# Kernel tuning notes

Hardware: AMD Instinct MI355X
Metric: run time of the kernel (lower is better)

## Reference

```python
import jax, jax.numpy as jnp
import numpy as np

SCALE, K, PATCH, STRIDE = 2, 5, 3, 1
EPS = 1e-5


def im2patch(x, p, s):
    # x: (b,c,H,W) -> (b,c,p,p,m1,m2), 'VALID' patches (padding is 0 for our sizes)
    b, c, H, W = x.shape
    m1 = (H - p) // s + 1
    m2 = (W - p) // s + 1
    ii = (jnp.arange(m1) * s)[:, None] + jnp.arange(p)[None, :]   # (m1,p)
    jj = (jnp.arange(m2) * s)[:, None] + jnp.arange(p)[None, :]   # (m2,p)
    pt = x[:, :, ii[:, :, None, None], jj[None, None, :, :]]      # (b,c,m1,p,m2,p)
    return pt.transpose(0, 1, 3, 5, 2, 4)                         # (b,c,p,p,m1,m2)


def patch2im(patches, p, s):
    # overlap-add fold, averaged by per-pixel patch counts (torch F.fold / ones-fold divisor)
    b, c, _, _, m1, m2 = patches.shape
    Hp = (m1 - 1) * s + p
    Wp = (m2 - 1) * s + p
    out = jnp.zeros((b, c, Hp, Wp), patches.dtype)
    cnt = jnp.zeros((Hp, Wp), patches.dtype)
    for i in range(p):          # fixed small loop over patch offsets (p*p = 36)
        for j in range(p):
            out = out.at[:, :, i:i + s * m1:s, j:j + s * m2:s].add(patches[:, :, i, j])
            cnt = cnt.at[i:i + s * m1:s, j:j + s * m2:s].add(1.0)
    return out / cnt


def setup_inputs():
    key = jax.random.key(0)
    k1, k2, k3 = jax.random.split(key, 3)
    b, cy, H, W = 1, 64, 80, 80
    y = jax.random.normal(k1, (b, cy, H, W), jnp.float32)
    yd = jax.random.normal(k2, (b, cy * SCALE ** 2, H // SCALE, W // SCALE), jnp.float32)
    m = ((H - PATCH) // STRIDE + 1) ** 2
    n = ((H // SCALE - PATCH) // STRIDE + 1) ** 2
    idx_k = jax.random.randint(k3, (b, m, K), 0, n, jnp.int32)
    return {"y": y, "yd": yd, "idx_k": idx_k}


def reference(y, yd, idx_k):
    b, cy, H, W = y.shape
    c = yd.shape[1]           # = cy * scale^2
    rs = SCALE ** 2
    y_p = im2patch(y, PATCH, STRIDE)      # (b,cy,p,p,m1,m2)
    yd_p = im2patch(yd, PATCH, STRIDE)    # (b,c,p,p,n1,n2)
    m1, m2 = y_p.shape[-2:]
    n1, n2 = yd_p.shape[-2:]
    m, n = m1 * m2, n1 * n2
    f = c * PATCH * PATCH
    y_flat = y_p.transpose(0, 4, 5, 1, 2, 3).reshape(b, m, f // rs)
    yd_flat = yd_p.transpose(0, 4, 5, 1, 2, 3).reshape(b, n, f)
    # top-k neighbor gather: (b,n,f)[idx (b,m,k)] -> (b,m,k,f) -> (b,m,f,k)
    z = jax.vmap(lambda t, i: t[i])(yd_flat, idx_k)
    z = z.transpose(0, 1, 3, 2)
    # AdaIN: normalize gathered HR patches, apply LR query patch stats (unbiased var, torch default)
    y_n = y_flat.reshape(b, m, c // rs, PATCH * PATCH)
    z_n = z.reshape(b, m, c // rs, rs * PATCH * PATCH, K)
    z_mu = z_n.mean(axis=3, keepdims=True)
    z_sd = jnp.sqrt(z_n.var(axis=3, ddof=1, keepdims=True) + EPS)
    y_mu = y_n.mean(axis=3, keepdims=True)[..., None]        # (b,m,c',1,1)
    y_sd = jnp.sqrt(y_n.var(axis=3, ddof=1, keepdims=True) + EPS)[..., None]
    z = ((z_n - z_mu) / z_sd * y_sd + y_mu).reshape(b, m, f, K)
    # rearrange f = (cy, scale, scale, p1, p2) into SR patches (b, k*cy, p*scale, p*scale, m1, m2)
    z = z.transpose(0, 3, 2, 1)                                   # (b,k,f,m)
    z = z.reshape(b, K, cy, SCALE, SCALE, PATCH, PATCH, m1, m2)
    z = z.transpose(0, 1, 2, 5, 3, 6, 4, 7, 8)                    # (b,k,cy,p1,s,p2,s,m1,m2)
    z = z.reshape(b, K * cy, PATCH * SCALE, PATCH * SCALE, m1, m2)
    z_sr = patch2im(z, PATCH * SCALE, STRIDE * SCALE)             # (b,k*cy,H*scale,W*scale)
    return z_sr.reshape(b, K * cy, H * SCALE, W * SCALE)
```

## Files before the change

### kernel.cpp

```cpp
#include <hip/hip_runtime.h>
#include <hip/hip_fp16.h>
#include <string.h>

#define CY     64
#define HY     80
#define HD     40
#define SPD    (HD*HD)
#define M1     78
#define N1     38
#define M_TOT  (M1*M1)
#define N_TOT  (N1*N1)
#define KK     5
#define HS     160
#define EPSF   1e-5f
#define LP     33

typedef float f32x2 __attribute__((ext_vector_type(2)));

__device__ __forceinline__ unsigned pkf16(float a, float b) {
    __half2 h = __floats2half2_rn(a, b);
    unsigned u; memcpy(&u, &h, 4); return u;
}
__device__ __forceinline__ f32x2 upk2(unsigned u) {
    __half2 h; memcpy(&h, &u, 4);
    float2 f = __half22float2(h);
    f32x2 r; r.x = f.x; r.y = f.y; return r;
}

__global__ __launch_bounds__(256) void pre_kernel(const float* __restrict__ y,
                                                  const float* __restrict__ yd,
                                                  uint4* __restrict__ ydW,
                                                  unsigned* __restrict__ zstP,
                                                  unsigned* __restrict__ ystP) {
    int id = blockIdx.x * 256 + threadIdx.x;
    if (id < SPD * 64) {
        int cc = id & 63, sp = id >> 6;
        const float* b0 = yd + (cc * 4) * SPD + sp;
        int d = (sp < SPD - 1) ? 1 : 0;
        ydW[sp * 64 + cc] = make_uint4(pkf16(b0[0], b0[SPD]),
                                       pkf16(b0[2*SPD], b0[3*SPD]),
                                       pkf16(b0[d], b0[SPD+d]),
                                       pkf16(b0[2*SPD+d], b0[3*SPD+d]));
        return;
    }
    id -= SPD * 64;
    if (id < N_TOT * 64) {
        int n  = id % N_TOT;
        int cc = id / N_TOT;
        int ni = n / N1, nj = n - ni * N1;
        const float* base = yd + (cc * 4) * SPD + ni * HD + nj;
        float s = 0.f, sq = 0.f;
#pragma unroll
        for (int r = 0; r < 4; ++r)
#pragma unroll
            for (int i = 0; i < 3; ++i)
#pragma unroll
                for (int j = 0; j < 3; ++j) {
                    float v = base[r * SPD + i * HD + j];
                    s += v; sq += v * v;
                }
        float mu  = s * (1.f / 36.f);
        float var = (sq - 36.f * mu * mu) * (1.f / 35.f);
        zstP[n * 64 + cc] = pkf16(mu, rsqrtf(var + EPSF));
        return;
    }
    id -= N_TOT * 64;
    if (id >= CY * M_TOT) return;
    int m  = id % M_TOT;
    int cc = id / M_TOT;
    int mi = m / M1, mj = m - mi * M1;
    const float* base = y + cc * (HY * HY) + mi * HY + mj;
    float s = 0.f, sq = 0.f;
#pragma unroll
    for (int i = 0; i < 3; ++i)
#pragma unroll
        for (int j = 0; j < 3; ++j) {
            float v = base[i * HY + j];
            s += v; sq += v * v;
        }
    float mu  = s * (1.f / 9.f);
    float var = (sq - 9.f * mu * mu) * (1.f / 8.f);
    ystP[m * 64 + cc] = pkf16(mu, sqrtf(var + EPSF));
}

__global__ __launch_bounds__(512) void agg_kernel(
    const uint4* __restrict__ ydW, const unsigned* __restrict__ zstP,
    const unsigned* __restrict__ ystP, const int* __restrict__ idx,
    float* __restrict__ out)
{
    __shared__ float lds[128 * LP];

    int lane = threadIdx.x & 63;
    int w    = __builtin_amdgcn_readfirstlane(threadIdx.x >> 6);
    int bid  = blockIdx.x;
    int wg   = (bid & 7) * 250 + (bid >> 3);
    int k    = wg / 400;
    int rem  = wg - k * 400;
    int y    = rem / 5;
    int xb2  = rem - y * 5;
    int x0   = xb2 * 16 + w * 2;

    f32x2 acc01[2] = {{0.f,0.f},{0.f,0.f}};
    f32x2 acc23[2] = {{0.f,0.f},{0.f,0.f}};
    float bs[2] = {0.f, 0.f};
    float inv0, inv1;

    auto serve = [&](f32x2& a01, f32x2& a23, float& bsum,
                     unsigned lo, unsigned hi, float a, float b) {
        f32x2 am; am.x = a; am.y = a;
        a01 = __builtin_elementwise_fma(am, upk2(lo), a01);
        a23 = __builtin_elementwise_fma(am, upk2(hi), a23);
        bsum += b;
    };

    if (y >= 2 && y <= M1 - 1 && x0 >= 2 && x0 <= M1 - 2) {
        inv0 = inv1 = 1.f / 9.f;
        unsigned ysu[12], zsu[12];
        int nn[12];
#pragma unroll
        for (int p = 0; p < 12; ++p) {
            int m = (y - 2 + (p >> 2)) * M1 + (x0 - 2 + (p & 3));
            nn[p]  = idx[m * KK + k];
            ysu[p] = ystP[m * 64 + lane];
        }
#pragma unroll
        for (int p = 0; p < 12; ++p)
            zsu[p] = zstP[nn[p] * 64 + lane];
        float aa[12], bb[12];
        int spb[12];
#pragma unroll
        for (int p = 0; p < 12; ++p) {
            f32x2 ys = upk2(ysu[p]), zs = upk2(zsu[p]);
            aa[p] = ys.y * zs.y;
            bb[p] = fmaf(-zs.x, aa[p], ys.x);
            int n = nn[p], ni = n / N1;
            spb[p] = ni * HD + (n - ni * N1);
        }
#pragma unroll
        for (int r = 0; r < 3; ++r) {
            int roff = (2 - r) * HD;
            int s0 = spb[r*4+0] + roff, s1 = spb[r*4+1] + roff;
            int s2 = spb[r*4+2] + roff, s3 = spb[r*4+3] + roff;
            uint2 v0 = *(const uint2*)(ydW + (s0 + 2) * 64 + lane);
            uint4 v1 = ydW[(s1 + 1) * 64 + lane];
            uint4 v2 = ydW[(s2 + 0) * 64 + lane];
            uint2 v3 = *(const uint2*)(ydW + (s3 + 0) * 64 + lane);
            serve(acc01[0], acc23[0], bs[0], v0.x, v0.y, aa[r*4+0], bb[r*4+0]);
            serve(acc01[0], acc23[0], bs[0], v1.x, v1.y, aa[r*4+1], bb[r*4+1]);
            serve(acc01[1], acc23[1], bs[1], v1.z, v1.w, aa[r*4+1], bb[r*4+1]);
            serve(acc01[0], acc23[0], bs[0], v2.x, v2.y, aa[r*4+2], bb[r*4+2]);
            serve(acc01[1], acc23[1], bs[1], v2.z, v2.w, aa[r*4+2], bb[r*4+2]);
            serve(acc01[1], acc23[1], bs[1], v3.x, v3.y, aa[r*4+3], bb[r*4+3]);
        }
    } else {
#pragma unroll
        for (int q = 0; q < 2; ++q) {
            int x = x0 + q;
            int milo = max(0, y - 2), mihi = min(M1 - 1, y);
            int mjlo = max(0, x - 2), mjhi = min(M1 - 1, x);
            float iv = 1.f / (float)((mihi - milo + 1) * (mjhi - mjlo + 1));
            if (q == 0) inv0 = iv; else inv1 = iv;
            for (int mi = milo; mi <= mihi; ++mi)
                for (int mj = mjlo; mj <= mjhi; ++mj) {
                    int m = mi * M1 + mj;
                    int n = idx[m * KK + k];
                    f32x2 ys = upk2(ystP[m * 64 + lane]);
                    f32x2 zs = upk2(zstP[n * 64 + lane]);
                    float a = ys.y * zs.y;
                    float b = fmaf(-zs.x, a, ys.x);
                    int ni = n / N1;
                    int sp = ni * HD + (n - ni * N1) + (y - mi) * HD + (x - mj);
                    uint2 v = *(const uint2*)(ydW + sp * 64 + lane);
                    if (q == 0) serve(acc01[0], acc23[0], bs[0], v.x, v.y, a, b);
                    else        serve(acc01[1], acc23[1], bs[1], v.x, v.y, a, b);
                }
        }
    }

#pragma unroll
    for (int q = 0; q < 2; ++q) {
        float iv = q ? inv1 : inv0;
        float bq = bs[q];
        int col = (w * 2 + q) * 2;
        lds[(0 * CY + lane) * LP + col]     = (acc01[q].x + bq) * iv;
        lds[(0 * CY + lane) * LP + col + 1] = (acc01[q].y + bq) * iv;
        lds[(1 * CY + lane) * LP + col]     = (acc23[q].x + bq) * iv;
        lds[(1 * CY + lane) * LP + col + 1] = (acc23[q].y + bq) * iv;
    }

    __syncthreads();

    int rsel = lane >> 5, c = lane & 31;
    int X0 = xb2 * 32, Y0 = 2 * y;
#pragma unroll
    for (int t = 0; t < 8; ++t) {
        int row = t * 16 + w * 2 + rsel;
        float v = lds[row * LP + c];
        int dy = row >> 6, cc = row & 63;
        out[((size_t)(k * CY + cc) * HS + (Y0 + dy)) * HS + X0 + c] = v;
    }
}

extern "C" void kernel_launch(void* const* d_in, const int* in_sizes, int n_in,
                              void* d_out, int out_size, void* d_ws, size_t ws_size,
                              hipStream_t stream) {
    const float* y   = (const float*)d_in[0];
    const float* yd  = (const float*)d_in[1];
    const int*   idx = (const int*)d_in[2];
    float* out = (float*)d_out;

    char* ws = (char*)d_ws;
    uint4*    ydW  = (uint4*)ws;
    unsigned* zstP = (unsigned*)(ws + 1638400);
    unsigned* ystP = (unsigned*)(ws + 2008064);

    int pre_total = SPD * 64 + N_TOT * 64 + CY * M_TOT;
    pre_kernel<<<(pre_total + 255) / 256, 256, 0, stream>>>(y, yd, ydW, zstP, ystP);
    agg_kernel<<<KK * 400, 512, 0, stream>>>(ydW, zstP, ystP, idx, out);
}
```

Baseline: 35.47 us.

## Compute four output columns per wave to reuse neighbor patch loads

```diff
diff --git a/kernel.cpp b/kernel.cpp
--- a/kernel.cpp
+++ b/kernel.cpp
@@ -83,7 +83,7 @@
     ystP[m * 64 + cc] = pkf16(mu, sqrtf(var + EPSF));
 }
 
-__global__ __launch_bounds__(512) void agg_kernel(
+__global__ __launch_bounds__(256) void agg_kernel(
     const uint4* __restrict__ ydW, const unsigned* __restrict__ zstP,
     const unsigned* __restrict__ ystP, const int* __restrict__ idx,
     float* __restrict__ out)
@@ -97,69 +97,77 @@
     int k    = wg / 400;
     int rem  = wg - k * 400;
     int y    = rem / 5;
-    int xb2  = rem - y * 5;
-    int x0   = xb2 * 16 + w * 2;
-
-    f32x2 acc01[2] = {{0.f,0.f},{0.f,0.f}};
-    f32x2 acc23[2] = {{0.f,0.f},{0.f,0.f}};
-    float bs[2] = {0.f, 0.f};
-    float inv0, inv1;
-
-    auto serve = [&](f32x2& a01, f32x2& a23, float& bsum,
-                     unsigned lo, unsigned hi, float a, float b) {
+    int xsb  = rem - y * 5;
+    int x0   = xsb * 16 + w * 4;
+
+    f32x2 acc01[4] = {{0.f,0.f},{0.f,0.f},{0.f,0.f},{0.f,0.f}};
+    f32x2 acc23[4] = {{0.f,0.f},{0.f,0.f},{0.f,0.f},{0.f,0.f}};
+    float bs[4]  = {0.f, 0.f, 0.f, 0.f};
+    float inv[4] = {1.f/9.f, 1.f/9.f, 1.f/9.f, 1.f/9.f};
+
+    auto serve = [&](int q, unsigned lo, unsigned hi, float a, float b) {
         f32x2 am; am.x = a; am.y = a;
-        a01 = __builtin_elementwise_fma(am, upk2(lo), a01);
-        a23 = __builtin_elementwise_fma(am, upk2(hi), a23);
-        bsum += b;
+        acc01[q] = __builtin_elementwise_fma(am, upk2(lo), acc01[q]);
+        acc23[q] = __builtin_elementwise_fma(am, upk2(hi), acc23[q]);
+        bs[q] += b;
     };
 
-    if (y >= 2 && y <= M1 - 1 && x0 >= 2 && x0 <= M1 - 2) {
-        inv0 = inv1 = 1.f / 9.f;
-        unsigned ysu[12], zsu[12];
-        int nn[12];
-#pragma unroll
-        for (int p = 0; p < 12; ++p) {
-            int m = (y - 2 + (p >> 2)) * M1 + (x0 - 2 + (p & 3));
-            nn[p]  = idx[m * KK + k];
-            ysu[p] = ystP[m * 64 + lane];
-        }
-#pragma unroll
-        for (int p = 0; p < 12; ++p)
-            zsu[p] = zstP[nn[p] * 64 + lane];
-        float aa[12], bb[12];
-        int spb[12];
-#pragma unroll
-        for (int p = 0; p < 12; ++p) {
-            f32x2 ys = upk2(ysu[p]), zs = upk2(zsu[p]);
-            aa[p] = ys.y * zs.y;
-            bb[p] = fmaf(-zs.x, aa[p], ys.x);
-            int n = nn[p], ni = n / N1;
-            spb[p] = ni * HD + (n - ni * N1);
+    if (y >= 2 && y <= M1 - 1 && x0 >= 2 && x0 + 3 <= M1 - 1) {
+        int nn[18];
+#pragma unroll
+        for (int p = 0; p < 18; ++p) {
+            int m = (y - 2 + p / 6) * M1 + (x0 - 2 + p % 6);
+            nn[p] = idx[m * KK + k];
         }
 #pragma unroll
         for (int r = 0; r < 3; ++r) {
-            int roff = (2 - r) * HD;
-            int s0 = spb[r*4+0] + roff, s1 = spb[r*4+1] + roff;
-            int s2 = spb[r*4+2] + roff, s3 = spb[r*4+3] + roff;
-            uint2 v0 = *(const uint2*)(ydW + (s0 + 2) * 64 + lane);
-            uint4 v1 = ydW[(s1 + 1) * 64 + lane];
-            uint4 v2 = ydW[(s2 + 0) * 64 + lane];
-            uint2 v3 = *(const uint2*)(ydW + (s3 + 0) * 64 + lane);
-            serve(acc01[0], acc23[0], bs[0], v0.x, v0.y, aa[r*4+0], bb[r*4+0]);
-            serve(acc01[0], acc23[0], bs[0], v1.x, v1.y, aa[r*4+1], bb[r*4+1]);
-            serve(acc01[1], acc23[1], bs[1], v1.z, v1.w, aa[r*4+1], bb[r*4+1]);
-            serve(acc01[0], acc23[0], bs[0], v2.x, v2.y, aa[r*4+2], bb[r*4+2]);
-            serve(acc01[1], acc23[1], bs[1], v2.z, v2.w, aa[r*4+2], bb[r*4+2]);
-            serve(acc01[1], acc23[1], bs[1], v3.x, v3.y, aa[r*4+3], bb[r*4+3]);
+            int roff  = (2 - r) * HD;
+            int base_m = (y - 2 + r) * M1 + (x0 - 2);
+            unsigned ysu[6], zsu[6];
+            int sp[6];
+#pragma unroll
+            for (int c = 0; c < 6; ++c) {
+                int n = nn[r * 6 + c];
+                ysu[c] = ystP[(base_m + c) * 64 + lane];
+                zsu[c] = zstP[n * 64 + lane];
+                int ni = n / N1;
+                sp[c]  = ni * HD + (n - ni * N1) + roff;
+            }
+            uint2 w0 = *(const uint2*)(ydW + (sp[0] + 2) * 64 + lane);
+            uint4 u1 = ydW[(sp[1] + 1) * 64 + lane];
+            uint4 u2 = ydW[(sp[2] + 0) * 64 + lane];
+            uint2 w2 = *(const uint2*)(ydW + (sp[2] + 2) * 64 + lane);
+            uint4 u3 = ydW[(sp[3] + 0) * 64 + lane];
+            uint2 w3 = *(const uint2*)(ydW + (sp[3] + 2) * 64 + lane);
+            uint4 u4 = ydW[(sp[4] + 0) * 64 + lane];
+            uint2 w5 = *(const uint2*)(ydW + (sp[5] + 0) * 64 + lane);
+            float aa[6], bb[6];
+#pragma unroll
+            for (int c = 0; c < 6; ++c) {
+                f32x2 ys = upk2(ysu[c]), zs = upk2(zsu[c]);
+                aa[c] = ys.y * zs.y;
+                bb[c] = fmaf(-zs.x, aa[c], ys.x);
+            }
+            serve(0, w0.x, w0.y, aa[0], bb[0]);
+            serve(0, u1.x, u1.y, aa[1], bb[1]);
+            serve(1, u1.z, u1.w, aa[1], bb[1]);
+            serve(0, u2.x, u2.y, aa[2], bb[2]);
+            serve(1, u2.z, u2.w, aa[2], bb[2]);
+            serve(2, w2.x, w2.y, aa[2], bb[2]);
+            serve(1, u3.x, u3.y, aa[3], bb[3]);
+            serve(2, u3.z, u3.w, aa[3], bb[3]);
+            serve(3, w3.x, w3.y, aa[3], bb[3]);
+            serve(2, u4.x, u4.y, aa[4], bb[4]);
+            serve(3, u4.z, u4.w, aa[4], bb[4]);
+            serve(3, w5.x, w5.y, aa[5], bb[5]);
         }
     } else {
 #pragma unroll
-        for (int q = 0; q < 2; ++q) {
+        for (int q = 0; q < 4; ++q) {
             int x = x0 + q;
             int milo = max(0, y - 2), mihi = min(M1 - 1, y);
             int mjlo = max(0, x - 2), mjhi = min(M1 - 1, x);
-            float iv = 1.f / (float)((mihi - milo + 1) * (mjhi - mjlo + 1));
-            if (q == 0) inv0 = iv; else inv1 = iv;
+            inv[q] = 1.f / (float)((mihi - milo + 1) * (mjhi - mjlo + 1));
             for (int mi = milo; mi <= mihi; ++mi)
                 for (int mj = mjlo; mj <= mjhi; ++mj) {
                     int m = mi * M1 + mj;
@@ -169,19 +177,18 @@
                     float a = ys.y * zs.y;
                     float b = fmaf(-zs.x, a, ys.x);
                     int ni = n / N1;
-                    int sp = ni * HD + (n - ni * N1) + (y - mi) * HD + (x - mj);
-                    uint2 v = *(const uint2*)(ydW + sp * 64 + lane);
-                    if (q == 0) serve(acc01[0], acc23[0], bs[0], v.x, v.y, a, b);
-                    else        serve(acc01[1], acc23[1], bs[1], v.x, v.y, a, b);
+                    int spq = ni * HD + (n - ni * N1) + (y - mi) * HD + (x - mj);
+                    uint2 v = *(const uint2*)(ydW + spq * 64 + lane);
+                    serve(q, v.x, v.y, a, b);
                 }
         }
     }
 
 #pragma unroll
-    for (int q = 0; q < 2; ++q) {
-        float iv = q ? inv1 : inv0;
+    for (int q = 0; q < 4; ++q) {
+        float iv = inv[q];
         float bq = bs[q];
-        int col = (w * 2 + q) * 2;
+        int col = w * 8 + q * 2;
         lds[(0 * CY + lane) * LP + col]     = (acc01[q].x + bq) * iv;
         lds[(0 * CY + lane) * LP + col + 1] = (acc01[q].y + bq) * iv;
         lds[(1 * CY + lane) * LP + col]     = (acc23[q].x + bq) * iv;
@@ -191,10 +198,10 @@
     __syncthreads();
 
     int rsel = lane >> 5, c = lane & 31;
-    int X0 = xb2 * 32, Y0 = 2 * y;
-#pragma unroll
-    for (int t = 0; t < 8; ++t) {
-        int row = t * 16 + w * 2 + rsel;
+    int X0 = xsb * 32, Y0 = 2 * y;
+#pragma unroll
+    for (int t = 0; t < 16; ++t) {
+        int row = t * 8 + w * 2 + rsel;
         float v = lds[row * LP + c];
         int dy = row >> 6, cc = row & 63;
         out[((size_t)(k * CY + cc) * HS + (Y0 + dy)) * HS + X0 + c] = v;
@@ -216,5 +223,5 @@
 
     int pre_total = SPD * 64 + N_TOT * 64 + CY * M_TOT;
     pre_kernel<<<(pre_total + 255) / 256, 256, 0, stream>>>(y, yd, ydW, zstP, ystP);
-    agg_kernel<<<KK * 400, 512, 0, stream>>>(ydW, zstP, ystP, idx, out);
-}
+    agg_kernel<<<KK * 400, 256, 0, stream>>>(ydW, zstP, ystP, idx, out);
+}
```

Result: slower. 40.08 us (+13.0%).
